# Kernel optimization log

Measured on AMD Instinct MI355X. Metric: run time of the kernel, lower is better.

## Reference

```python
import jax, jax.numpy as jnp
import numpy as np

BN_EPS = 1e-5
D_SLICE = 3  # forward slices last (neighbor) dim to :3 (d=3 in original code)


def _conv_bn_relu(x, W, b, gamma, beta):
    # x: (B, Cin, N, K) ; W: (Cout, Cin) ; 1x1 Conv2d + eval-mode BatchNorm(mean=0, var=1) + ReLU
    y = jnp.einsum('oi,bink->bonk', W, x) + b[:, None, None]
    y = gamma[:, None, None] * (y / jnp.sqrt(1.0 + BN_EPS)) + beta[:, None, None]
    return jax.nn.relu(y)


def setup_inputs() -> dict:
    key = jax.random.key(0)
    ks = jax.random.split(key, 16)
    B, N, K, C = 4, 32768, 16, 64
    mlp = [128, 64, 64]
    cin = C + 4  # feature + relation (diff_xyz 3 + distance 1)
    inp = {
        'src_xyz': jax.random.normal(ks[0], (B, 3, N, K), dtype=jnp.float32),
        'tgt_xyz': jax.random.normal(ks[1], (B, 3, N), dtype=jnp.float32),
        'feature': jax.random.normal(ks[2], (B, C, N, K), dtype=jnp.float32),
    }
    c_prev = cin
    for i, c_out in enumerate(mlp):
        scale = 1.0 / np.sqrt(c_prev)
        inp[f'W{i+1}'] = jax.random.uniform(ks[3 + 4 * i], (c_out, c_prev), minval=-scale, maxval=scale, dtype=jnp.float32)
        inp[f'b{i+1}'] = jax.random.uniform(ks[4 + 4 * i], (c_out,), minval=-scale, maxval=scale, dtype=jnp.float32)
        inp[f'g{i+1}'] = jnp.ones((c_out,), dtype=jnp.float32)
        inp[f'be{i+1}'] = jnp.zeros((c_out,), dtype=jnp.float32)
        c_prev = c_out
    return inp


def reference(src_xyz, tgt_xyz, feature, W1, b1, g1, be1, W2, b2, g2, be2, W3, b3, g3, be3):
    # relation feature on first D_SLICE neighbors (faithful to feature[:,:,:,:d], d=3)
    diff_xyz = src_xyz[:, :, :, :D_SLICE] - tgt_xyz[:, :, :, None]        # (B,3,N,3)
    distance = jnp.sum(diff_xyz ** 2, axis=1, keepdims=True)             # (B,1,N,3)
    x = jnp.concatenate([feature[:, :, :, :D_SLICE], diff_xyz, distance], axis=1)  # (B,C+4,N,3)
    x = _conv_bn_relu(x, W1, b1, g1, be1)
    x = _conv_bn_relu(x, W2, b2, g2, be2)
    x = _conv_bn_relu(x, W3, b3, g3, be3)
    return jnp.sum(x, axis=3)  # reduction='sum' over neighbor dim -> (B,64,N)
```

## Files before the change

kernel.cpp:

```cpp
#include <hip/hip_runtime.h>
#include <math.h>

typedef __attribute__((ext_vector_type(8))) short short8;
typedef __attribute__((ext_vector_type(4))) short short4v;
typedef __attribute__((ext_vector_type(4))) float f32x4;
typedef __attribute__((ext_vector_type(16))) float f32x16;
typedef _Float16 half8 __attribute__((ext_vector_type(8)));

constexpr int BLOCK = 512;
constexpr int B_ = 4, C_ = 64, N_ = 32768, K_ = 16;
constexpr int P_ = 32;
constexpr int NFRAG = 44;
constexpr int BIAS_OFF = NFRAG * 1024;

constexpr int ZOFF = 9 * 768;
constexpr int XSZ  = 6920;
constexpr int H2STR = 776;

__device__ __forceinline__ short f16bits(float v) {
    return (short)__builtin_bit_cast(unsigned short, (_Float16)v);
}

__device__ __forceinline__ f32x16 mm32h(half8 a, half8 b, f32x16 c) {
    return __builtin_amdgcn_mfma_f32_32x32x16_f16(a, b, c, 0, 0, 0);
}
__device__ __forceinline__ f32x4 mm16h(half8 a, half8 b, f32x4 c) {
    return __builtin_amdgcn_mfma_f32_16x16x32_f16(a, b, c, 0, 0, 0);
}

__global__ void prep_wfrags(const float* __restrict__ W1, const float* __restrict__ g1,
                            const float* __restrict__ b1, const float* __restrict__ be1,
                            const float* __restrict__ W2, const float* __restrict__ g2,
                            const float* __restrict__ b2, const float* __restrict__ be2,
                            const float* __restrict__ W3, const float* __restrict__ g3,
                            const float* __restrict__ b3, const float* __restrict__ be3,
                            unsigned short* __restrict__ wf)
{
    const int gid = blockIdx.x * 256 + threadIdx.x;
    const float RS = 1.0f / sqrtf(1.0f + 1e-5f);
    const int NT = NFRAG * 64;
    if (gid < NT) {
        const int f = gid >> 6, l = gid & 63;
        const float *W, *g; int CI, co, kb;
        if (f < 20)      { W = W1; g = g1; CI = 68;
                           co = (f / 5) * 32 + (l & 31);        kb = (f % 5) * 16 + (l >> 5) * 8; }
        else if (f < 36) { W = W2; g = g2; CI = 128;
                           co = ((f - 20) / 8) * 32 + (l & 31); kb = ((f - 20) % 8) * 16 + (l >> 5) * 8; }
        else             { W = W3; g = g3; CI = 64;
                           co = ((f - 36) / 2) * 16 + (l & 15); kb = ((f - 36) % 2) * 32 + (l >> 4) * 8; }
        const float gs = g[co] * RS;
        short8 h8, l8;
#pragma unroll
        for (int j = 0; j < 8; ++j) {
            const int k = kb + j;
            const float w = (k < CI) ? W[(size_t)co * CI + k] * gs : 0.0f;
            _Float16 hf = (_Float16)w;
            h8[j] = (short)__builtin_bit_cast(unsigned short, hf);
            l8[j] = f16bits(w - (float)hf);
        }
        *reinterpret_cast<short8*>(wf + (size_t)f * 1024 + l * 8)       = h8;
        *reinterpret_cast<short8*>(wf + (size_t)f * 1024 + 512 + l * 8) = l8;
    } else if (gid < NT + 256) {
        const int c = gid - NT;
        float* fb = reinterpret_cast<float*>(wf + BIAS_OFF);
        if (c < 128)      fb[c] = b1[c] * (g1[c] * RS) + be1[c];
        else if (c < 192) { const int q = c - 128; fb[c] = b2[q] * (g2[q] * RS) + be2[q]; }
        else              { const int q = c - 192; fb[c] = b3[q] * (g3[q] * RS) + be3[q]; }
    }
}

__device__ __forceinline__ void ldfrag(const unsigned short* __restrict__ wf,
                                       int f, int l, half8 &h, half8 &lo) {
    h  = __builtin_bit_cast(half8,
         *reinterpret_cast<const short8*>(wf + (size_t)f * 1024 + l * 8));
    lo = __builtin_bit_cast(half8,
         *reinterpret_cast<const short8*>(wf + (size_t)f * 1024 + 512 + l * 8));
}

__global__ __launch_bounds__(BLOCK, 6)
void mvp_mfma(const float* __restrict__ src, const float* __restrict__ tgt,
              const float* __restrict__ feat,
              const unsigned short* __restrict__ wf,
              float* __restrict__ out)
{
    __shared__ __align__(16) unsigned short xa[XSZ];
    __shared__ __align__(16) unsigned short h1f[16*768];

    const int tid = threadIdx.x;
    const int w   = tid >> 6;
    const int l   = tid & 63;
    const int b   = blockIdx.x >> 10;
    const int n0  = (blockIdx.x & 1023) << 5;

    unsigned short* h2f = xa;

    float4 pf[4];
#pragma unroll
    for (int it = 0; it < 4; ++it) {
        const int idx = tid + it * BLOCK;
        const int c = idx >> 5, p = idx & 31;
        pf[it] = *reinterpret_cast<const float4*>(
            feat + ((size_t)(b*C_ + c) * N_ + (n0 + p)) * K_);
    }
    float rl[6];
    if (tid < 96) {
        const int p = tid & 31, k = tid >> 5, n = n0 + p;
        rl[0] = src[((size_t)(b*3+0)*N_ + n)*K_ + k];
        rl[1] = src[((size_t)(b*3+1)*N_ + n)*K_ + k];
        rl[2] = src[((size_t)(b*3+2)*N_ + n)*K_ + k];
        rl[3] = tgt[(size_t)(b*3+0)*N_ + n];
        rl[4] = tgt[(size_t)(b*3+1)*N_ + n];
        rl[5] = tgt[(size_t)(b*3+2)*N_ + n];
    }

    if (tid < 96) {
        const int o = (8*96 + tid) * 8 + 4;
        *reinterpret_cast<short4v*>(&xa[o]) = short4v{0,0,0,0};
    } else if (tid == 96) {
        *reinterpret_cast<short8*>(xa + ZOFF) = short8{0,0,0,0,0,0,0,0};
    }

#pragma unroll
    for (int it = 0; it < 4; ++it) {
        const int idx = tid + it * BLOCK;
        const int c = idx >> 5, p = idx & 31;
        const float v[3] = {pf[it].x, pf[it].y, pf[it].z};
#pragma unroll
        for (int k = 0; k < 3; ++k)
            xa[((c >> 3)*96 + k*32 + p)*8 + (c & 7)] = (unsigned short)f16bits(v[k]);
    }
    if (tid < 96) {
        const int p = tid & 31, k = tid >> 5;
        const float d0 = rl[0]-rl[3], d1 = rl[1]-rl[4], d2 = rl[2]-rl[5];
        const float d[4] = {d0, d1, d2, d0*d0 + d1*d1 + d2*d2};
        const int base = (8*96 + k*32 + p)*8;
#pragma unroll
        for (int j = 0; j < 4; ++j)
            xa[base + j] = (unsigned short)f16bits(d[j]);
    }
    __syncthreads();

    const int hi32 = l >> 5, c32 = l & 31;
    const int lq = l >> 4, lr = l & 15, rq = lq << 2;
    const float* fb = reinterpret_cast<const float*>(wf + BIAS_OFF);

    {
        const int npass = (w < 4) ? 2 : 1;
        for (int pass = 0; pass < npass; ++pass) {
            const int t = pass ? (8 + w) : w;
            const int m = t / 3, n = t % 3;
            const int col = n*32 + c32;
            half8 ah[5], al[5];
#pragma unroll
            for (int ks = 0; ks < 5; ++ks) ldfrag(wf, m*5 + ks, l, ah[ks], al[ks]);
            f32x16 acc;
#pragma unroll
            for (int j = 0; j < 16; ++j) acc[j] = 0.0f;
#pragma unroll
            for (int ks = 0; ks < 4; ++ks) {
                const int so = ((ks*2 + hi32)*96 + col)*8;
                const half8 bh = __builtin_bit_cast(half8,
                    *reinterpret_cast<const short8*>(&xa[so]));
                acc = mm32h(ah[ks], bh, acc);
                acc = mm32h(al[ks], bh, acc);
            }
            {
                const int so = hi32 ? ZOFF : (8*96 + col)*8;
                const half8 bh = __builtin_bit_cast(half8,
                    *reinterpret_cast<const short8*>(&xa[so]));
                acc = mm32h(ah[4], bh, acc);
                acc = mm32h(al[4], bh, acc);
            }
#pragma unroll
            for (int g = 0; g < 4; ++g) {
                const int co0 = m*32 + 8*g + 4*hi32;
                const float4 bb = *reinterpret_cast<const float4*>(fb + co0);
                const float bbv[4] = {bb.x, bb.y, bb.z, bb.w};
                short4v h4;
#pragma unroll
                for (int r = 0; r < 4; ++r)
                    h4[r] = f16bits(fmaxf(acc[g*4 + r] + bbv[r], 0.0f));
                const int so = ((m*4 + g)*96 + col)*8 + 4*hi32;
                *reinterpret_cast<short4v*>(&h1f[so]) = h4;
            }
        }
    }
    __syncthreads();

    if (w < 6) {
        const int m = w / 3, n = w % 3;
        const int col = n*32 + c32;
        f32x16 acc;
#pragma unroll
        for (int j = 0; j < 16; ++j) acc[j] = 0.0f;
#pragma unroll
        for (int ks = 0; ks < 8; ++ks) {
            half8 ah, al;
            ldfrag(wf, 20 + m*8 + ks, l, ah, al);
            const int so = ((ks*2 + hi32)*96 + col)*8;
            const half8 bh = __builtin_bit_cast(half8,
                *reinterpret_cast<const short8*>(&h1f[so]));
            acc = mm32h(ah, bh, acc);
            acc = mm32h(al, bh, acc);
        }
#pragma unroll
        for (int g = 0; g < 4; ++g) {
            const int co0 = m*32 + 8*g + 4*hi32;
            const float4 bb = *reinterpret_cast<const float4*>(fb + 128 + co0);
            const float bbv[4] = {bb.x, bb.y, bb.z, bb.w};
            short4v h4;
#pragma unroll
            for (int r = 0; r < 4; ++r)
                h4[r] = f16bits(fmaxf(acc[g*4 + r] + bbv[r], 0.0f));
            const int so = (m*4 + g)*H2STR + col*8 + 4*hi32;
            *reinterpret_cast<short4v*>(&h2f[so]) = h4;
        }
    }
    __syncthreads();

    {
        const int m = w >> 1, hh = w & 1;
        half8 ah[2], al[2];
#pragma unroll
        for (int ks = 0; ks < 2; ++ks) ldfrag(wf, 36 + m*2 + ks, l, ah[ks], al[ks]);
        f32x4 acc3[3] = {f32x4{0,0,0,0}, f32x4{0,0,0,0}, f32x4{0,0,0,0}};
#pragma unroll
        for (int ks = 0; ks < 2; ++ks) {
#pragma unroll
            for (int t = 0; t < 3; ++t) {
                const int so = (ks*4 + lq)*H2STR + (t*32 + hh*16 + lr)*8;
                const half8 bh = __builtin_bit_cast(half8,
                    *reinterpret_cast<const short8*>(&h2f[so]));
                acc3[t] = mm16h(ah[ks], bh, acc3[t]);
                acc3[t] = mm16h(al[ks], bh, acc3[t]);
            }
        }
        const int co0 = m*16 + rq;
        const float4 bb = *reinterpret_cast<const float4*>(fb + 192 + co0);
        const float bbv[4] = {bb.x, bb.y, bb.z, bb.w};
#pragma unroll
        for (int r = 0; r < 4; ++r) {
            float s = 0.0f;
#pragma unroll
            for (int t = 0; t < 3; ++t) s += fmaxf(acc3[t][r] + bbv[r], 0.0f);
            out[(size_t)(b*64 + co0 + r) * N_ + n0 + hh*16 + lr] = s;
        }
    }
}

extern "C" void kernel_launch(void* const* d_in, const int* in_sizes, int n_in,
                              void* d_out, int out_size, void* d_ws, size_t ws_size,
                              hipStream_t stream) {
    const float* src  = (const float*)d_in[0];
    const float* tgt  = (const float*)d_in[1];
    const float* feat = (const float*)d_in[2];
    const float* W1 = (const float*)d_in[3];
    const float* b1 = (const float*)d_in[4];
    const float* g1 = (const float*)d_in[5];
    const float* be1= (const float*)d_in[6];
    const float* W2 = (const float*)d_in[7];
    const float* b2 = (const float*)d_in[8];
    const float* g2 = (const float*)d_in[9];
    const float* be2= (const float*)d_in[10];
    const float* W3 = (const float*)d_in[11];
    const float* b3 = (const float*)d_in[12];
    const float* g3 = (const float*)d_in[13];
    const float* be3= (const float*)d_in[14];
    float* out = (float*)d_out;
    unsigned short* wfrag = (unsigned short*)d_ws;

    prep_wfrags<<<12, 256, 0, stream>>>(W1, g1, b1, be1, W2, g2, b2, be2,
                                        W3, g3, b3, be3, wfrag);

    const int grid = B_ * (N_ / P_);
    mvp_mfma<<<grid, BLOCK, 0, stream>>>(src, tgt, feat, wfrag, out);
}
```

Before: 140.2 us.

## Double points per block to 64 and reuse weight fragments across column tiles

Each block now handles 64 points instead of 32, so shared-memory buffers double and the grid is halved. In layers 1 and 2 every wave keeps several accumulators and loads each weight fragment once, applying it across multiple 32-column tiles. This removes the repeated global/L2 weight-fragment loads and the uneven two-pass split in layer 1. In exchange, register pressure and LDS use per block rise, which may reduce occupancy under the 6-block launch bound.

```diff
diff --git a/kernel.cpp b/kernel.cpp
--- a/kernel.cpp
+++ b/kernel.cpp
@@ -9,13 +9,14 @@
 
 constexpr int BLOCK = 512;
 constexpr int B_ = 4, C_ = 64, N_ = 32768, K_ = 16;
-constexpr int P_ = 32;
+constexpr int P_ = 64;
+constexpr int NCOL = 192;
 constexpr int NFRAG = 44;
 constexpr int BIAS_OFF = NFRAG * 1024;
 
-constexpr int ZOFF = 9 * 768;
-constexpr int XSZ  = 6920;
-constexpr int H2STR = 776;
+constexpr int ZOFF = 9 * 1536;
+constexpr int XSZ  = 13832;
+constexpr int H2STR = 1544;
 
 __device__ __forceinline__ short f16bits(float v) {
     return (short)__builtin_bit_cast(unsigned short, (_Float16)v);
@@ -84,27 +85,25 @@
               float* __restrict__ out)
 {
     __shared__ __align__(16) unsigned short xa[XSZ];
-    __shared__ __align__(16) unsigned short h1f[16*768];
+    __shared__ __align__(16) unsigned short h1f[16*1536];
 
     const int tid = threadIdx.x;
     const int w   = tid >> 6;
     const int l   = tid & 63;
-    const int b   = blockIdx.x >> 10;
-    const int n0  = (blockIdx.x & 1023) << 5;
+    const int b   = blockIdx.x >> 9;
+    const int n0  = (blockIdx.x & 511) << 6;
 
     unsigned short* h2f = xa;
 
-    float4 pf[4];
-#pragma unroll
-    for (int it = 0; it < 4; ++it) {
-        const int idx = tid + it * BLOCK;
-        const int c = idx >> 5, p = idx & 31;
-        pf[it] = *reinterpret_cast<const float4*>(
-            feat + ((size_t)(b*C_ + c) * N_ + (n0 + p)) * K_);
+    if (tid < 192) {
+        const int o = (8*192 + tid) * 8 + 4;
+        *reinterpret_cast<short4v*>(&xa[o]) = short4v{0,0,0,0};
+    } else if (tid == 192) {
+        *reinterpret_cast<short8*>(xa + ZOFF) = short8{0,0,0,0,0,0,0,0};
     }
     float rl[6];
-    if (tid < 96) {
-        const int p = tid & 31, k = tid >> 5, n = n0 + p;
+    if (tid < 192) {
+        const int p = tid & 63, k = tid >> 6, n = n0 + p;
         rl[0] = src[((size_t)(b*3+0)*N_ + n)*K_ + k];
         rl[1] = src[((size_t)(b*3+1)*N_ + n)*K_ + k];
         rl[2] = src[((size_t)(b*3+2)*N_ + n)*K_ + k];
@@ -112,28 +111,31 @@
         rl[4] = tgt[(size_t)(b*3+1)*N_ + n];
         rl[5] = tgt[(size_t)(b*3+2)*N_ + n];
     }
-
-    if (tid < 96) {
-        const int o = (8*96 + tid) * 8 + 4;
-        *reinterpret_cast<short4v*>(&xa[o]) = short4v{0,0,0,0};
-    } else if (tid == 96) {
-        *reinterpret_cast<short8*>(xa + ZOFF) = short8{0,0,0,0,0,0,0,0};
-    }
-
-#pragma unroll
-    for (int it = 0; it < 4; ++it) {
-        const int idx = tid + it * BLOCK;
-        const int c = idx >> 5, p = idx & 31;
-        const float v[3] = {pf[it].x, pf[it].y, pf[it].z};
-#pragma unroll
-        for (int k = 0; k < 3; ++k)
-            xa[((c >> 3)*96 + k*32 + p)*8 + (c & 7)] = (unsigned short)f16bits(v[k]);
-    }
-    if (tid < 96) {
-        const int p = tid & 31, k = tid >> 5;
+#pragma unroll
+    for (int grp = 0; grp < 2; ++grp) {
+        float4 pf[4];
+#pragma unroll
+        for (int it = 0; it < 4; ++it) {
+            const int idx = tid + (grp*4 + it) * BLOCK;
+            const int c = idx >> 6, p = idx & 63;
+            pf[it] = *reinterpret_cast<const float4*>(
+                feat + ((size_t)(b*C_ + c) * N_ + (n0 + p)) * K_);
+        }
+#pragma unroll
+        for (int it = 0; it < 4; ++it) {
+            const int idx = tid + (grp*4 + it) * BLOCK;
+            const int c = idx >> 6, p = idx & 63;
+            const float v[3] = {pf[it].x, pf[it].y, pf[it].z};
+#pragma unroll
+            for (int k = 0; k < 3; ++k)
+                xa[((c >> 3)*192 + k*64 + p)*8 + (c & 7)] = (unsigned short)f16bits(v[k]);
+        }
+    }
+    if (tid < 192) {
+        const int p = tid & 63, k = tid >> 6;
         const float d0 = rl[0]-rl[3], d1 = rl[1]-rl[4], d2 = rl[2]-rl[5];
         const float d[4] = {d0, d1, d2, d0*d0 + d1*d1 + d2*d2};
-        const int base = (8*96 + k*32 + p)*8;
+        const int base = (8*192 + k*64 + p)*8;
 #pragma unroll
         for (int j = 0; j < 4; ++j)
             xa[base + j] = (unsigned short)f16bits(d[j]);
@@ -145,32 +147,31 @@
     const float* fb = reinterpret_cast<const float*>(wf + BIAS_OFF);
 
     {
-        const int npass = (w < 4) ? 2 : 1;
-        for (int pass = 0; pass < npass; ++pass) {
-            const int t = pass ? (8 + w) : w;
-            const int m = t / 3, n = t % 3;
-            const int col = n*32 + c32;
-            half8 ah[5], al[5];
-#pragma unroll
-            for (int ks = 0; ks < 5; ++ks) ldfrag(wf, m*5 + ks, l, ah[ks], al[ks]);
-            f32x16 acc;
-#pragma unroll
-            for (int j = 0; j < 16; ++j) acc[j] = 0.0f;
-#pragma unroll
-            for (int ks = 0; ks < 4; ++ks) {
-                const int so = ((ks*2 + hi32)*96 + col)*8;
+        const int m = w >> 1, nh = w & 1;
+        f32x16 acc[3];
+#pragma unroll
+        for (int nn = 0; nn < 3; ++nn)
+#pragma unroll
+            for (int j = 0; j < 16; ++j) acc[nn][j] = 0.0f;
+
+#pragma unroll
+        for (int ks = 0; ks < 5; ++ks) {
+            half8 ah, al;
+            ldfrag(wf, m*5 + ks, l, ah, al);
+#pragma unroll
+            for (int nn = 0; nn < 3; ++nn) {
+                const int col = (nh*3 + nn)*32 + c32;
+                const int so = (ks < 4) ? ((ks*2 + hi32)*192 + col)*8
+                                        : (hi32 ? ZOFF : (8*192 + col)*8);
                 const half8 bh = __builtin_bit_cast(half8,
                     *reinterpret_cast<const short8*>(&xa[so]));
-                acc = mm32h(ah[ks], bh, acc);
-                acc = mm32h(al[ks], bh, acc);
-            }
-            {
-                const int so = hi32 ? ZOFF : (8*96 + col)*8;
-                const half8 bh = __builtin_bit_cast(half8,
-                    *reinterpret_cast<const short8*>(&xa[so]));
-                acc = mm32h(ah[4], bh, acc);
-                acc = mm32h(al[4], bh, acc);
-            }
+                acc[nn] = mm32h(ah, bh, acc[nn]);
+                acc[nn] = mm32h(al, bh, acc[nn]);
+            }
+        }
+#pragma unroll
+        for (int nn = 0; nn < 3; ++nn) {
+            const int col = (nh*3 + nn)*32 + c32;
 #pragma unroll
             for (int g = 0; g < 4; ++g) {
                 const int co0 = m*32 + 8*g + 4*hi32;
@@ -179,8 +180,8 @@
                 short4v h4;
 #pragma unroll
                 for (int r = 0; r < 4; ++r)
-                    h4[r] = f16bits(fmaxf(acc[g*4 + r] + bbv[r], 0.0f));
-                const int so = ((m*4 + g)*96 + col)*8 + 4*hi32;
+                    h4[r] = f16bits(fmaxf(acc[nn][g*4 + r] + bbv[r], 0.0f));
+                const int so = ((m*4 + g)*192 + col)*8 + 4*hi32;
                 *reinterpret_cast<short4v*>(&h1f[so]) = h4;
             }
         }
@@ -188,62 +189,76 @@
     __syncthreads();
 
     if (w < 6) {
-        const int m = w / 3, n = w % 3;
-        const int col = n*32 + c32;
-        f32x16 acc;
-#pragma unroll
-        for (int j = 0; j < 16; ++j) acc[j] = 0.0f;
+        const int m = w / 3, np = w % 3;
+        f32x16 acc[2];
+#pragma unroll
+        for (int nn = 0; nn < 2; ++nn)
+#pragma unroll
+            for (int j = 0; j < 16; ++j) acc[nn][j] = 0.0f;
+
 #pragma unroll
         for (int ks = 0; ks < 8; ++ks) {
             half8 ah, al;
             ldfrag(wf, 20 + m*8 + ks, l, ah, al);
-            const int so = ((ks*2 + hi32)*96 + col)*8;
-            const half8 bh = __builtin_bit_cast(half8,
-                *reinterpret_cast<const short8*>(&h1f[so]));
-            acc = mm32h(ah, bh, acc);
-            acc = mm32h(al, bh, acc);
-        }
-#pragma unroll
-        for (int g = 0; g < 4; ++g) {
-            const int co0 = m*32 + 8*g + 4*hi32;
-            const float4 bb = *reinterpret_cast<const float4*>(fb + 128 + co0);
+#pragma unroll
+            for (int nn = 0; nn < 2; ++nn) {
+                const int col = (np*2 + nn)*32 + c32;
+                const int so = ((ks*2 + hi32)*192 + col)*8;
+                const half8 bh = __builtin_bit_cast(half8,
+                    *reinterpret_cast<const short8*>(&h1f[so]));
+                acc[nn] = mm32h(ah, bh, acc[nn]);
+                acc[nn] = mm32h(al, bh, acc[nn]);
+            }
+        }
+#pragma unroll
+        for (int nn = 0; nn < 2; ++nn) {
+            const int col = (np*2 + nn)*32 + c32;
+#pragma unroll
+            for (int g = 0; g < 4; ++g) {
+                const int co0 = m*32 + 8*g + 4*hi32;
+                const float4 bb = *reinterpret_cast<const float4*>(fb + 128 + co0);
+                const float bbv[4] = {bb.x, bb.y, bb.z, bb.w};
+                short4v h4;
+#pragma unroll
+                for (int r = 0; r < 4; ++r)
+                    h4[r] = f16bits(fmaxf(acc[nn][g*4 + r] + bbv[r], 0.0f));
+                const int so = (m*4 + g)*H2STR + col*8 + 4*hi32;
+                *reinterpret_cast<short4v*>(&h2f[so]) = h4;
+            }
+        }
+    }
+    __syncthreads();
+
+    {
+        const int m = w >> 1;
+        half8 ah[2], al[2];
+#pragma unroll
+        for (int ks = 0; ks < 2; ++ks) ldfrag(wf, 36 + m*2 + ks, l, ah[ks], al[ks]);
+#pragma unroll
+        for (int pass = 0; pass < 2; ++pass) {
+            const int pq = (w & 1)*2 + pass;
+            f32x4 acc3[3] = {f32x4{0,0,0,0}, f32x4{0,0,0,0}, f32x4{0,0,0,0}};
+#pragma unroll
+            for (int ks = 0; ks < 2; ++ks) {
+#pragma unroll
+                for (int t = 0; t < 3; ++t) {
+                    const int so = (ks*4 + lq)*H2STR + (t*64 + pq*16 + lr)*8;
+                    const half8 bh = __builtin_bit_cast(half8,
+                        *reinterpret_cast<const short8*>(&h2f[so]));
+                    acc3[t] = mm16h(ah[ks], bh, acc3[t]);
+                    acc3[t] = mm16h(al[ks], bh, acc3[t]);
+                }
+            }
+            const int co0 = m*16 + rq;
+            const float4 bb = *reinterpret_cast<const float4*>(fb + 192 + co0);
             const float bbv[4] = {bb.x, bb.y, bb.z, bb.w};
-            short4v h4;
-#pragma unroll
-            for (int r = 0; r < 4; ++r)
-                h4[r] = f16bits(fmaxf(acc[g*4 + r] + bbv[r], 0.0f));
-            const int so = (m*4 + g)*H2STR + col*8 + 4*hi32;
-            *reinterpret_cast<short4v*>(&h2f[so]) = h4;
-        }
-    }
-    __syncthreads();
-
-    {
-        const int m = w >> 1, hh = w & 1;
-        half8 ah[2], al[2];
-#pragma unroll
-        for (int ks = 0; ks < 2; ++ks) ldfrag(wf, 36 + m*2 + ks, l, ah[ks], al[ks]);
-        f32x4 acc3[3] = {f32x4{0,0,0,0}, f32x4{0,0,0,0}, f32x4{0,0,0,0}};
-#pragma unroll
-        for (int ks = 0; ks < 2; ++ks) {
-#pragma unroll
-            for (int t = 0; t < 3; ++t) {
-                const int so = (ks*4 + lq)*H2STR + (t*32 + hh*16 + lr)*8;
-                const half8 bh = __builtin_bit_cast(half8,
-                    *reinterpret_cast<const short8*>(&h2f[so]));
-                acc3[t] = mm16h(ah[ks], bh, acc3[t]);
-                acc3[t] = mm16h(al[ks], bh, acc3[t]);
-            }
-        }
-        const int co0 = m*16 + rq;
-        const float4 bb = *reinterpret_cast<const float4*>(fb + 192 + co0);
-        const float bbv[4] = {bb.x, bb.y, bb.z, bb.w};
-#pragma unroll
-        for (int r = 0; r < 4; ++r) {
-            float s = 0.0f;
-#pragma unroll
-            for (int t = 0; t < 3; ++t) s += fmaxf(acc3[t][r] + bbv[r], 0.0f);
-            out[(size_t)(b*64 + co0 + r) * N_ + n0 + hh*16 + lr] = s;
+#pragma unroll
+            for (int r = 0; r < 4; ++r) {
+                float s = 0.0f;
+#pragma unroll
+                for (int t = 0; t < 3; ++t) s += fmaxf(acc3[t][r] + bbv[r], 0.0f);
+                out[(size_t)(b*64 + co0 + r) * N_ + n0 + pq*16 + lr] = s;
+            }
         }
     }
 }
```

After: 148.0 us. +5.6%, slower.
